# Performance work log

Measured on AMD Instinct MI355X. Metric: run time of the kernel, lower is better.

The kernel has to match this reference:

```python
import jax, jax.numpy as jnp
import numpy as np

H_DIM = 2048
D_FF = 4 * H_DIM
NUM_EXPERTS = 8
NUM_SHARED = 2
BATCH, SEQ = 2, 2048


def setup_inputs() -> dict:
    key = jax.random.key(0)
    ks = jax.random.split(key, 10)
    s = 0.02
    return {
        "x": jax.random.normal(ks[0], (BATCH, SEQ, H_DIM), dtype=jnp.float32),
        "ws_w1": jax.random.normal(ks[1], (NUM_SHARED, H_DIM, D_FF), dtype=jnp.float32) * s,
        "ws_b1": jnp.zeros((NUM_SHARED, D_FF), dtype=jnp.float32),
        "ws_w2": jax.random.normal(ks[2], (NUM_SHARED, D_FF, H_DIM), dtype=jnp.float32) * s,
        "ws_b2": jnp.zeros((NUM_SHARED, H_DIM), dtype=jnp.float32),
        "we_w1": jax.random.normal(ks[3], (NUM_EXPERTS, H_DIM, D_FF), dtype=jnp.float32) * s,
        "we_b1": jnp.zeros((NUM_EXPERTS, D_FF), dtype=jnp.float32),
        "we_w2": jax.random.normal(ks[4], (NUM_EXPERTS, D_FF, H_DIM), dtype=jnp.float32) * s,
        "we_b2": jnp.zeros((NUM_EXPERTS, H_DIM), dtype=jnp.float32),
        "wg": jax.random.normal(ks[5], (H_DIM, NUM_EXPERTS), dtype=jnp.float32) * s,
        "top_k": 2,
    }


def reference(x, ws_w1, ws_b1, ws_w2, ws_b2, we_w1, we_b1, we_w2, we_b2, wg, top_k):
    B, S, D = x.shape
    xt = x.reshape(-1, D)  # [T, D], T = B*S
    T = xt.shape[0]

    # ---- shared experts: sum over NUM_SHARED dense MLPs ----
    hs = jax.nn.relu(jnp.einsum('td,ndf->ntf', xt, ws_w1) + ws_b1[:, None, :])
    shared = jnp.einsum('ntf,nfd->td', hs, ws_w2) + ws_b2.sum(axis=0)  # [T, D]

    # ---- sparse top-k routed MoE ----
    logits = xt @ wg                       # [T, E] router logits
    probs = jax.nn.softmax(logits, axis=-1)
    topv, topi = jax.lax.top_k(probs, top_k)
    gates = jnp.zeros_like(probs).at[jnp.arange(T)[:, None], topi].set(topv)  # [T, E]

    moe = jnp.zeros_like(xt)
    for e in range(we_w1.shape[0]):  # small fixed expert count
        he = jax.nn.relu(xt @ we_w1[e] + we_b1[e])
        ye = he @ we_w2[e] + we_b2[e]
        moe = moe + gates[:, e:e + 1] * ye

    out = (shared + moe).reshape(B, S, D)
    return out, logits
```

## Files before the change

kernel.cpp:

```cpp
#include <hip/hip_runtime.h>

#define TOKENS 4096
#define HD 2048
#define FF 8192
#define NE 8
#define NS 2

typedef __attribute__((ext_vector_type(8))) short bf16x8;
typedef __attribute__((ext_vector_type(4))) float f32x4;

__device__ __forceinline__ unsigned rnd_bf(unsigned u) {
  return u + 0x7fffu + ((u >> 16) & 1u);
}
__device__ __forceinline__ unsigned short f2bf(float f) {
  unsigned u = __builtin_bit_cast(unsigned, f);
  return (unsigned short)(rnd_bf(u) >> 16);
}

#define GLDS16(gp, lp)                                                         \
  __builtin_amdgcn_global_load_lds(                                            \
      (const __attribute__((address_space(1))) unsigned*)(const void*)(gp),    \
      (__attribute__((address_space(3))) unsigned*)(lp), 16, 0, 0)

__global__ void cast_x_kernel(const float* __restrict__ x, unsigned short* __restrict__ xb) {
  const size_t i = ((size_t)blockIdx.x * 256 + threadIdx.x) * 4;
  float4 v = *(const float4*)(x + i);
  ushort4 o;
  o.x = f2bf(v.x); o.y = f2bf(v.y); o.z = f2bf(v.z); o.w = f2bf(v.w);
  *(ushort4*)(xb + i) = o;
}

__global__ void router_kernel(const float* __restrict__ x, const float* __restrict__ wg,
                              float* __restrict__ logits_out, int* __restrict__ topi,
                              float* __restrict__ topv, int* __restrict__ counts) {
  const int wave = threadIdx.x >> 6, lane = threadIdx.x & 63;
  const int t = blockIdx.x * 4 + wave;
  const float* xr = x + (size_t)t * HD;
  float acc[8];
#pragma unroll
  for (int e = 0; e < 8; ++e) acc[e] = 0.f;
  for (int d = lane; d < HD; d += 64) {
    const float xv = xr[d];
    const float4 w0 = *(const float4*)(wg + (size_t)d * 8);
    const float4 w1 = *(const float4*)(wg + (size_t)d * 8 + 4);
    acc[0] += xv * w0.x; acc[1] += xv * w0.y; acc[2] += xv * w0.z; acc[3] += xv * w0.w;
    acc[4] += xv * w1.x; acc[5] += xv * w1.y; acc[6] += xv * w1.z; acc[7] += xv * w1.w;
  }
#pragma unroll
  for (int e = 0; e < 8; ++e) {
#pragma unroll
    for (int off = 32; off > 0; off >>= 1) acc[e] += __shfl_xor(acc[e], off);
  }
  if (lane == 0) {
    *(float4*)(logits_out + (size_t)t * 8)     = make_float4(acc[0], acc[1], acc[2], acc[3]);
    *(float4*)(logits_out + (size_t)t * 8 + 4) = make_float4(acc[4], acc[5], acc[6], acc[7]);
    float mx = acc[0];
#pragma unroll
    for (int e = 1; e < 8; ++e) mx = fmaxf(mx, acc[e]);
    float p[8], s = 0.f;
#pragma unroll
    for (int e = 0; e < 8; ++e) { p[e] = expf(acc[e] - mx); s += p[e]; }
    const float inv = 1.f / s;
    int i1 = 0;
#pragma unroll
    for (int e = 1; e < 8; ++e) if (acc[e] > acc[i1]) i1 = e;
    int i2 = (i1 == 0) ? 1 : 0;
#pragma unroll
    for (int e = 0; e < 8; ++e) if (e != i1 && acc[e] > acc[i2]) i2 = e;
    topi[2 * t]     = i1; topv[2 * t]     = p[i1] * inv;
    topi[2 * t + 1] = i2; topv[2 * t + 1] = p[i2] * inv;
    atomicAdd(&counts[i1], 1);
    atomicAdd(&counts[i2], 1);
  }
}

__global__ void offs_kernel(const int* __restrict__ counts, int* __restrict__ offs,
                            int* __restrict__ cursors) {
  if (threadIdx.x == 0) {
    int r = 0;
    for (int e = 0; e < NE; ++e) { offs[e] = r; cursors[e] = r; r += counts[e]; }
  }
}

__global__ void gather_kernel(const unsigned short* __restrict__ xb,
                              const int* __restrict__ topi, const float* __restrict__ topv,
                              int* __restrict__ cursors, unsigned short* __restrict__ xg,
                              int* __restrict__ row_token, float* __restrict__ row_gate,
                              int* __restrict__ row_of) {
  const int wave = threadIdx.x >> 6, lane = threadIdx.x & 63;
  const int t = blockIdx.x * 4 + wave;
  const uint4* src = (const uint4*)(xb + (size_t)t * HD);
#pragma unroll
  for (int j = 0; j < 2; ++j) {
    const int e = topi[2 * t + j];
    int pos = 0;
    if (lane == 0) {
      pos = atomicAdd(&cursors[e], 1);
      row_token[pos] = t;
      row_gate[pos] = topv[2 * t + j];
      row_of[2 * t + j] = pos;
    }
    pos = __shfl(pos, 0);
    uint4* dst = (uint4*)(xg + (size_t)pos * HD);
#pragma unroll
    for (int c = lane; c < 256; c += 64) dst[c] = src[c];
  }
}

template <int K, int N>
__global__ __launch_bounds__(256) void pack_wt(const float* __restrict__ we,
                                               const float* __restrict__ ws,
                                               unsigned short* __restrict__ dstw) {
  const int e = blockIdx.z;
  const float* src = (e < NE) ? (we + (size_t)e * K * N) : (ws + (size_t)(e - NE) * K * N);
  unsigned short* dst = dstw + (size_t)e * K * N;
  const int nt = blockIdx.x * 64;
  const int kt = blockIdx.y * 64;
  __shared__ unsigned short t[64][73];
  const int tid = threadIdx.x;
  const int rr = tid >> 4, cc = (tid & 15) * 4;
#pragma unroll
  for (int i = 0; i < 4; ++i) {
    const int k = rr + i * 16;
    float4 v = *(const float4*)(src + (size_t)(kt + k) * N + nt + cc);
    t[k][cc + 0] = f2bf(v.x);
    t[k][cc + 1] = f2bf(v.y);
    t[k][cc + 2] = f2bf(v.z);
    t[k][cc + 3] = f2bf(v.w);
  }
  __syncthreads();
  const int nr = tid >> 2, kc = (tid & 3) * 16;
  unsigned u[8];
#pragma unroll
  for (int j = 0; j < 8; ++j)
    u[j] = (unsigned)t[kc + 2 * j][nr] | ((unsigned)t[kc + 2 * j + 1][nr] << 16);
  unsigned short* dp = dst + (size_t)(nt + nr) * K + kt + kc;
  uint4 v0; v0.x = u[0]; v0.y = u[1]; v0.z = u[2]; v0.w = u[3];
  uint4 v1; v1.x = u[4]; v1.y = u[5]; v1.z = u[6]; v1.w = u[7];
  *(uint4*)dp = v0;
  *(uint4*)(dp + 8) = v1;
}

template <int MS>
__device__ __forceinline__ void rd_a(bf16x8 (&d)[8], const unsigned short* base,
                                     int wr, int fr, int fq, int swz) {
#pragma unroll
  for (int mi = 0; mi < 4; ++mi)
#pragma unroll
    for (int ks = 0; ks < 2; ++ks)
      d[mi * 2 + ks] = *(const bf16x8*)(base + (wr * 128 + MS * 64 + mi * 16 + fr) * 64 +
                                        (((ks * 4 + fq) ^ swz) << 3));
}
template <int NSUB>
__device__ __forceinline__ void rd_b(bf16x8 (&d)[4], const unsigned short* base,
                                     int wc, int fr, int fq, int swz) {
#pragma unroll
  for (int ni = 0; ni < 2; ++ni)
#pragma unroll
    for (int ks = 0; ks < 2; ++ks)
      d[ni * 2 + ks] = *(const bf16x8*)(base + (wc * 64 + NSUB * 32 + ni * 16 + fr) * 64 +
                                        (((ks * 4 + fq) ^ swz) << 3));
}
template <int MS, int NSUB>
__device__ __forceinline__ void mm16(f32x4 (&acc)[8][4], const bf16x8 (&a)[8],
                                     const bf16x8 (&b)[4]) {
  __builtin_amdgcn_s_setprio(1);
#pragma unroll
  for (int mi = 0; mi < 4; ++mi)
#pragma unroll
    for (int ni = 0; ni < 2; ++ni)
#pragma unroll
      for (int ks = 0; ks < 2; ++ks)
        acc[MS * 4 + mi][NSUB * 2 + ni] = __builtin_amdgcn_mfma_f32_16x16x32_bf16(
            a[mi * 2 + ks], b[ni * 2 + ks], acc[MS * 4 + mi][NSUB * 2 + ni], 0, 0, 0);
  __builtin_amdgcn_s_setprio(0);
}
template <int MS>
__device__ __forceinline__ void mm32(f32x4 (&acc)[8][4], const bf16x8 (&a)[8],
                                     const bf16x8 (&b0)[4], const bf16x8 (&b1)[4]) {
  __builtin_amdgcn_s_setprio(1);
#pragma unroll
  for (int mi = 0; mi < 4; ++mi)
#pragma unroll
    for (int nn = 0; nn < 4; ++nn)
#pragma unroll
      for (int ks = 0; ks < 2; ++ks) {
        const bf16x8& bb = (nn < 2) ? b0[(nn & 1) * 2 + ks] : b1[(nn & 1) * 2 + ks];
        acc[MS * 4 + mi][nn] = __builtin_amdgcn_mfma_f32_16x16x32_bf16(
            a[mi * 2 + ks], bb, acc[MS * 4 + mi][nn], 0, 0, 0);
      }
  __builtin_amdgcn_s_setprio(0);
}

#define PH_BAR_PRE()                                                           \
  __builtin_amdgcn_sched_barrier(0);                                           \
  __builtin_amdgcn_s_barrier();                                                \
  asm volatile("s_waitcnt lgkmcnt(0)" ::: "memory");                           \
  __builtin_amdgcn_sched_barrier(0)
#define PH_BAR_POST()                                                          \
  __builtin_amdgcn_sched_barrier(0);                                           \
  __builtin_amdgcn_s_barrier()

__global__ __launch_bounds__(512, 2) void g1k(
    const unsigned short* __restrict__ Ash, const unsigned short* __restrict__ Art,
    const unsigned short* __restrict__ wt1,
    const float* __restrict__ bE, const float* __restrict__ bS,
    unsigned short* __restrict__ hout,
    const int* __restrict__ counts, const int* __restrict__ offs,
    int do_pack, const float* __restrict__ we_w2, const float* __restrict__ ws_w2,
    unsigned short* __restrict__ wt2) {
  constexpr int K = HD;
  constexpr int NBX = FF / 256;
  constexpr int NWG = NBX * 16;
  extern __shared__ unsigned short smem[];

  const int e = blockIdx.z;
  int M;
  const unsigned short* A;
  const float* bias;
  int hbase;
  if (e < NE) {
    M = counts[e];
    A = Art + (size_t)offs[e] * K;
    bias = bE + (size_t)e * FF;
    hbase = offs[e];
  } else {
    M = TOKENS;
    A = Ash;
    bias = bS + (size_t)(e - NE) * FF;
    hbase = 2 * TOKENS + (e - NE) * TOKENS;
  }
  const unsigned short* Bt = wt1 + (size_t)e * HD * FF;

  int flat = blockIdx.x + NBX * blockIdx.y;
  flat = (flat & 7) * (NWG >> 3) + (flat >> 3);
  const int m0 = (flat & 15) * 256;
  const int n0 = (flat >> 4) * 256;
  const int tid = threadIdx.x;

  if (m0 >= M) {
    if (!do_pack) return;
    int total = 0, prefix = 0;
    for (int e2 = 0; e2 < NE; ++e2) {
      int mb = (counts[e2] + 255) >> 8; if (mb > 16) mb = 16;
      const int inv = 32 * (16 - mb);
      if (e2 < e) prefix += inv;
      total += inv;
    }
    int mb_e = (counts[e] + 255) >> 8; if (mb_e > 16) mb_e = 16;
    const int m_idx = flat & 15, n_idx = flat >> 4;
    const int rank = prefix + n_idx * (16 - mb_e) + (m_idx - mb_e);
    unsigned short* ps = smem;
    const int NT = 10 * 128 * 32;
    for (int i = rank; i < NT; i += total) {
      const int e2 = i >> 12;
      const int rem = i & 4095;
      const int ktt = rem >> 5;
      const int ntt = rem & 31;
      const float* src = (e2 < NE) ? (we_w2 + (size_t)e2 * FF * HD)
                                   : (ws_w2 + (size_t)(e2 - NE) * FF * HD);
      unsigned short* dst = wt2 + (size_t)e2 * HD * FF;
      __syncthreads();
      {
        const int kk = tid >> 3, cc = (tid & 7) * 8;
        const float* sp = src + (size_t)(ktt * 64 + kk) * HD + ntt * 64 + cc;
        const float4 v0 = *(const float4*)sp;
        const float4 v1 = *(const float4*)(sp + 4);
        unsigned short* tp = ps + kk * 72 + cc;
        tp[0] = f2bf(v0.x); tp[1] = f2bf(v0.y); tp[2] = f2bf(v0.z); tp[3] = f2bf(v0.w);
        tp[4] = f2bf(v1.x); tp[5] = f2bf(v1.y); tp[6] = f2bf(v1.z); tp[7] = f2bf(v1.w);
      }
      __syncthreads();
      {
        const int nn = tid >> 3, kc = (tid & 7) * 8;
        unsigned u[4];
#pragma unroll
        for (int j = 0; j < 4; ++j)
          u[j] = (unsigned)ps[(kc + 2 * j) * 72 + nn] |
                 ((unsigned)ps[(kc + 2 * j + 1) * 72 + nn] << 16);
        uint4 v; v.x = u[0]; v.y = u[1]; v.z = u[2]; v.w = u[3];
        *(uint4*)(dst + (size_t)(ntt * 64 + nn) * FF + ktt * 64 + kc) = v;
      }
    }
    return;
  }

  const int wid = tid >> 6, ln = tid & 63;
  const int wr = wid >> 2, wc = wid & 3;
  const int fr = ln & 15, fq = ln >> 4;
  const int swz = fr & 7;
  const int lr8 = ln >> 3;
  const int lc8 = ln & 7;
  const int scol = (lc8 ^ lr8) << 3;
  const int wrA = wr * 128 + wc * 16;
  const int wcB = wc * 64 + wr * 16;

#define SA1(s, kt, b)                                                          \
  { const int r0_ = wrA + (s) * 64 + lr8;                                      \
    const unsigned short* s_ = A + (size_t)(m0 + r0_) * K + (kt) * 64 + scol;  \
    unsigned short* d_ = smem + (b) * 32768 + r0_ * 64 + lc8 * 8;              \
    GLDS16(s_, d_); GLDS16(s_ + (size_t)8 * K, d_ + 8 * 64); }
#define SB1(s, kt, b)                                                          \
  { const int r0_ = wcB + (s) * 32 + lr8;                                      \
    const unsigned short* s_ = Bt + (size_t)(n0 + r0_) * K + (kt) * 64 + scol; \
    unsigned short* d_ = smem + (b) * 32768 + 16384 + r0_ * 64 + lc8 * 8;      \
    GLDS16(s_, d_); GLDS16(s_ + (size_t)8 * K, d_ + 8 * 64); }

  f32x4 acc[8][4];
#pragma unroll
  for (int i = 0; i < 8; ++i)
#pragma unroll
    for (int j = 0; j < 4; ++j) acc[i][j] = (f32x4){0.f, 0.f, 0.f, 0.f};

  SA1(0, 0, 0); SA1(1, 0, 0); SB1(0, 0, 0); SB1(1, 0, 0);
  SA1(0, 1, 1); SA1(1, 1, 1); SB1(0, 1, 1); SB1(1, 1, 1);
  asm volatile("s_waitcnt vmcnt(8)" ::: "memory");
  __builtin_amdgcn_s_barrier();

  bf16x8 a0[8], a1[8], b0[4], b1[4];
  const int nkt = K / 64;
  for (int t = 0; t < nkt; ++t) {
    const int cur = t & 1;
    const int tp2 = (t + 2 < nkt) ? t + 2 : t;
    const unsigned short* As_c = smem + cur * 32768;
    const unsigned short* Bs_c = As_c + 16384;
    rd_a<0>(a0, As_c, wr, fr, fq, swz);
    rd_b<0>(b0, Bs_c, wc, fr, fq, swz);
    rd_b<1>(b1, Bs_c, wc, fr, fq, swz);
    asm volatile("s_waitcnt lgkmcnt(8)" ::: "memory");
    PH_BAR_PRE();
    mm32<0>(acc, a0, b0, b1);
    PH_BAR_POST();
    rd_a<1>(a1, As_c, wr, fr, fq, swz);
    SB1(0, tp2, cur); SB1(1, tp2, cur);
    PH_BAR_PRE();
    mm32<1>(acc, a1, b1, b0);
    __builtin_amdgcn_sched_barrier(0);
    SA1(0, tp2, cur); SA1(1, tp2, cur);
    __builtin_amdgcn_sched_barrier(0);
    asm volatile("s_waitcnt vmcnt(8)" ::: "memory");
    __builtin_amdgcn_s_barrier();
  }
#undef SA1
#undef SB1

#pragma unroll
  for (int nn = 0; nn < 4; ++nn) {
#pragma unroll
    for (int mm = 0; mm < 8; ++mm) {
      const int nsub_lo = (mm < 4) ? (nn >> 1) : 1 - (nn >> 1);
      const int col = n0 + wc * 64 + nsub_lo * 32 + (nn & 1) * 16 + fr;
      const float bb = bias[col];
#pragma unroll
      for (int j = 0; j < 4; ++j) {
        const int r = m0 + wr * 128 + (mm >> 2) * 64 + (mm & 3) * 16 + fq * 4 + j;
        if (r < M) {
          float v = acc[mm][nn][j] + bb;
          v = v > 0.f ? v : 0.f;
          hout[(size_t)(hbase + r) * FF + col] = f2bf(v);
        }
      }
    }
  }
}

__global__ __launch_bounds__(512, 2) void g2k(
    const unsigned short* __restrict__ hbuf, const unsigned short* __restrict__ wt2,
    const float* __restrict__ bE, const float* __restrict__ bS,
    float* __restrict__ ybuf,
    const int* __restrict__ counts, const int* __restrict__ offs) {
  constexpr int K = FF;
  constexpr int NBX = HD / 256;
  constexpr int NWG = NBX * 16;
  extern __shared__ unsigned short smem[];

  const int e = blockIdx.z;
  int M;
  const unsigned short* A;
  const float* bias;
  int hbase;
  if (e < NE) {
    M = counts[e];
    A = hbuf + (size_t)offs[e] * K;
    bias = bE + (size_t)e * HD;
    hbase = offs[e];
  } else {
    M = TOKENS;
    hbase = 2 * TOKENS + (e - NE) * TOKENS;
    A = hbuf + (size_t)hbase * K;
    bias = bS + (size_t)(e - NE) * HD;
  }
  const unsigned short* Bt = wt2 + (size_t)e * HD * FF;

  int flat = blockIdx.x + NBX * blockIdx.y;
  flat = (flat & 7) * (NWG >> 3) + (flat >> 3);
  const int m0 = (flat & 15) * 256;
  const int n0 = (flat >> 4) * 256;
  if (m0 >= M) return;

  const int tid = threadIdx.x;
  const int wid = tid >> 6, ln = tid & 63;
  const int wr = wid >> 2, wc = wid & 3;
  const int fr = ln & 15, fq = ln >> 4;
  const int swz = fr & 7;
  const int lr8 = ln >> 3;
  const int lc8 = ln & 7;
  const int scol = (lc8 ^ lr8) << 3;
  const int wrA = wr * 128 + wc * 16;
  const int wcB = wc * 64 + wr * 16;

#define SA2(s, kt, b)                                                          \
  { const int r0_ = wrA + (s) * 64 + lr8;                                      \
    const unsigned short* s_ = A + (size_t)(m0 + r0_) * K + (kt) * 64 + scol;  \
    unsigned short* d_ = smem + (b) * 32768 + r0_ * 64 + lc8 * 8;              \
    GLDS16(s_, d_); GLDS16(s_ + (size_t)8 * K, d_ + 8 * 64); }
#define SB2(s, kt, b)                                                          \
  { const int r0_ = wcB + (s) * 32 + lr8;                                      \
    const unsigned short* s_ = Bt + (size_t)(n0 + r0_) * K + (kt) * 64 + scol; \
    unsigned short* d_ = smem + (b) * 32768 + 16384 + r0_ * 64 + lc8 * 8;      \
    GLDS16(s_, d_); GLDS16(s_ + (size_t)8 * K, d_ + 8 * 64); }

  f32x4 acc[8][4];
#pragma unroll
  for (int i = 0; i < 8; ++i)
#pragma unroll
    for (int j = 0; j < 4; ++j) acc[i][j] = (f32x4){0.f, 0.f, 0.f, 0.f};

  SA2(0, 0, 0); SA2(1, 0, 0); SB2(0, 0, 0); SB2(1, 0, 0);
  SA2(0, 1, 1); SA2(1, 1, 1); SB2(0, 1, 1); SB2(1, 1, 1);
  asm volatile("s_waitcnt vmcnt(8)" ::: "memory");
  __builtin_amdgcn_s_barrier();

  bf16x8 a0[8], a1[8], b0[4], b1[4];
  const int nkt = K / 64;
  for (int t = 0; t < nkt; ++t) {
    const int cur = t & 1;
    const int tp2 = (t + 2 < nkt) ? t + 2 : t;
    const unsigned short* As_c = smem + cur * 32768;
    const unsigned short* Bs_c = As_c + 16384;
    rd_a<0>(a0, As_c, wr, fr, fq, swz);
    rd_b<0>(b0, Bs_c, wc, fr, fq, swz);
    rd_b<1>(b1, Bs_c, wc, fr, fq, swz);
    asm volatile("s_waitcnt lgkmcnt(8)" ::: "memory");
    PH_BAR_PRE();
    mm32<0>(acc, a0, b0, b1);
    PH_BAR_POST();
    rd_a<1>(a1, As_c, wr, fr, fq, swz);
    SB2(0, tp2, cur); SB2(1, tp2, cur);
    PH_BAR_PRE();
    mm32<1>(acc, a1, b1, b0);
    __builtin_amdgcn_sched_barrier(0);
    SA2(0, tp2, cur); SA2(1, tp2, cur);
    __builtin_amdgcn_sched_barrier(0);
    asm volatile("s_waitcnt vmcnt(8)" ::: "memory");
    __builtin_amdgcn_s_barrier();
  }
#undef SA2
#undef SB2

#pragma unroll
  for (int nn = 0; nn < 4; ++nn) {
#pragma unroll
    for (int mm = 0; mm < 8; ++mm) {
      const int nsub_lo = (mm < 4) ? (nn >> 1) : 1 - (nn >> 1);
      const int colw = wc * 64 + nsub_lo * 32 + (nn & 1) * 16 + fr;
      const float bb = bias[n0 + colw];
#pragma unroll
      for (int j = 0; j < 4; ++j) {
        const int r = m0 + wr * 128 + (mm >> 2) * 64 + (mm & 3) * 16 + fq * 4 + j;
        if (r < M)
          ybuf[(size_t)(hbase + r) * HD + n0 + colw] = acc[mm][nn][j] + bb;
      }
    }
  }
}

__global__ __launch_bounds__(256) void reduce_kernel(
    const float* __restrict__ ybuf, const int* __restrict__ row_of,
    const float* __restrict__ topv, float* __restrict__ out) {
  const int t = blockIdx.x;
  const int d = threadIdx.x * 8;
  const float g0 = topv[2 * t], g1 = topv[2 * t + 1];
  const float* y0 = ybuf + (size_t)row_of[2 * t] * HD + d;
  const float* y1 = ybuf + (size_t)row_of[2 * t + 1] * HD + d;
  const float* s0 = ybuf + (size_t)(2 * TOKENS + t) * HD + d;
  const float* s1 = ybuf + (size_t)(3 * TOKENS + t) * HD + d;
  float* o = out + (size_t)t * HD + d;
#pragma unroll
  for (int q = 0; q < 2; ++q) {
    const float4 a = *(const float4*)(s0 + q * 4);
    const float4 b = *(const float4*)(s1 + q * 4);
    const float4 c = *(const float4*)(y0 + q * 4);
    const float4 e = *(const float4*)(y1 + q * 4);
    float4 r;
    r.x = a.x + b.x + g0 * c.x + g1 * e.x;
    r.y = a.y + b.y + g0 * c.y + g1 * e.y;
    r.z = a.z + b.z + g0 * c.z + g1 * e.z;
    r.w = a.w + b.w + g0 * c.w + g1 * e.w;
    *(float4*)(o + q * 4) = r;
  }
}

__global__ __launch_bounds__(512, 2) void gemm8p(
    const unsigned short* __restrict__ hbuf,
    const unsigned short* __restrict__ wt,
    const float* __restrict__ bE, const float* __restrict__ bS,
    float* __restrict__ out,
    const int* __restrict__ counts, const int* __restrict__ offs,
    const int* __restrict__ row_token, const float* __restrict__ row_gate) {
  constexpr int K = FF;
  constexpr int NBX = HD / 256;
  constexpr int NWG = NBX * 16;
  extern __shared__ unsigned short smem[];

  const int e = blockIdx.z;
  const bool merged = (e == NE);
  int M;
  const unsigned short *A, *A2;
  const unsigned short *B, *B2;
  const float *bias, *bias2;
  const int* tok = nullptr;
  const float* gt = nullptr;

  if (!merged) {
    M = counts[e];
    const int off = offs[e];
    A = hbuf + (size_t)off * K;  A2 = A;
    tok = row_token + off; gt = row_gate + off;
    B = wt + (size_t)e * HD * FF;  B2 = B;
    bias = bE + (size_t)e * HD;  bias2 = bias;
  } else {
    M = TOKENS;
    A  = hbuf + (size_t)(2 * TOKENS) * K;
    A2 = hbuf + (size_t)(3 * TOKENS) * K;
    B  = wt + (size_t)NE * HD * FF;
    B2 = wt + (size_t)(NE + 1) * HD * FF;
    bias = bS;  bias2 = bS + HD;
  }

  int flat = blockIdx.x + NBX * blockIdx.y;
  flat = (flat & 7) * (NWG >> 3) + (flat >> 3);
  const int m0 = (flat & 15) * 256;
  const int n0 = (flat >> 4) * 256;
  if (m0 >= M) return;

  const int tid = threadIdx.x;
  const int wid = tid >> 6, ln = tid & 63;
  const int wr = wid >> 2, wc = wid & 3;
  const int fr = ln & 15, fq = ln >> 4;
  const int swz = fr & 7;
  const int lr8 = ln >> 3;
  const int lc8 = ln & 7;
  const int scol = (lc8 ^ lr8) << 3;
  const int wrA = wr * 128 + wc * 16;
  const int wcB = wc * 64 + wr * 16;

#define SAF(s, kt, b)                                                          \
  { int kl_ = (kt); const unsigned short* ab_ = A;                             \
    if (merged && kl_ >= 128) { ab_ = A2; kl_ -= 128; }                        \
    const int r0_ = wrA + (s) * 64 + lr8;                                      \
    const unsigned short* s_ = ab_ + (size_t)(m0 + r0_) * K + kl_ * 64 + scol; \
    unsigned short* d_ = smem + (b) * 32768 + r0_ * 64 + lc8 * 8;              \
    GLDS16(s_, d_); GLDS16(s_ + (size_t)8 * K, d_ + 8 * 64); }
#define SBF(s, kt, b)                                                          \
  { int kl_ = (kt); const unsigned short* bb_ = B;                             \
    if (merged && kl_ >= 128) { bb_ = B2; kl_ -= 128; }                        \
    const int r0_ = wcB + (s) * 32 + lr8;                                      \
    const unsigned short* s_ = bb_ + (size_t)(n0 + r0_) * K + kl_ * 64 + scol; \
    unsigned short* d_ = smem + (b) * 32768 + 16384 + r0_ * 64 + lc8 * 8;      \
    GLDS16(s_, d_); GLDS16(s_ + (size_t)8 * K, d_ + 8 * 64); }

  f32x4 acc[8][4];
#pragma unroll
  for (int i = 0; i < 8; ++i)
#pragma unroll
    for (int j = 0; j < 4; ++j) acc[i][j] = (f32x4){0.f, 0.f, 0.f, 0.f};

  SAF(0, 0, 0); SAF(1, 0, 0); SBF(0, 0, 0); SBF(1, 0, 0);
  SAF(0, 1, 1); SAF(1, 1, 1); SBF(0, 1, 1); SBF(1, 1, 1);
  asm volatile("s_waitcnt vmcnt(8)" ::: "memory");
  __builtin_amdgcn_s_barrier();

  bf16x8 a0[8], a1[8], b0[4], b1[4];
  const int nkt = merged ? 256 : 128;
  for (int t = 0; t < nkt; ++t) {
    const int cur = t & 1;
    const int tp2 = (t + 2 < nkt) ? t + 2 : t;
    const unsigned short* As_c = smem + cur * 32768;
    const unsigned short* Bs_c = As_c + 16384;
    rd_a<0>(a0, As_c, wr, fr, fq, swz);
    rd_b<0>(b0, Bs_c, wc, fr, fq, swz);
    asm volatile("s_waitcnt lgkmcnt(8)" ::: "memory");
    PH_BAR_PRE();
    mm16<0, 0>(acc, a0, b0);
    PH_BAR_POST();
    rd_b<1>(b1, Bs_c, wc, fr, fq, swz);
    SAF(0, tp2, cur); SBF(0, tp2, cur);
    PH_BAR_PRE();
    mm16<0, 1>(acc, a0, b1);
    PH_BAR_POST();
    rd_a<1>(a1, As_c, wr, fr, fq, swz);
    SBF(1, tp2, cur);
    PH_BAR_PRE();
    mm16<1, 1>(acc, a1, b1);
    PH_BAR_POST();
    SAF(1, tp2, cur);
    __builtin_amdgcn_sched_barrier(0);
    __builtin_amdgcn_s_barrier();
    __builtin_amdgcn_sched_barrier(0);
    mm16<1, 0>(acc, a1, b0);
    __builtin_amdgcn_sched_barrier(0);
    asm volatile("s_waitcnt vmcnt(8)" ::: "memory");
    __builtin_amdgcn_s_barrier();
  }
#undef SAF
#undef SBF

#pragma unroll
  for (int mm = 0; mm < 8; ++mm) {
#pragma unroll
    for (int j = 0; j < 4; ++j) {
      const int r = m0 + wr * 128 + (mm >> 2) * 64 + (mm & 3) * 16 + fq * 4 + j;
      if (r < M) {
        const int t = tok ? tok[r] : r;
        const float g = gt ? gt[r] : 1.f;
        float* orow = out + (size_t)t * HD + n0;
#pragma unroll
        for (int nn = 0; nn < 4; ++nn) {
          const int col = wc * 64 + (nn >> 1) * 32 + (nn & 1) * 16 + fr;
          float bb = bias[n0 + col];
          if (merged) bb += bias2[n0 + col];
          atomicAdd(orow + col, g * (acc[mm][nn][j] + bb));
        }
      }
    }
  }
}

extern "C" void kernel_launch(void* const* d_in, const int* in_sizes, int n_in,
                              void* d_out, int out_size, void* d_ws, size_t ws_size,
                              hipStream_t stream) {
  const float* x     = (const float*)d_in[0];
  const float* ws_w1 = (const float*)d_in[1];
  const float* ws_b1 = (const float*)d_in[2];
  const float* ws_w2 = (const float*)d_in[3];
  const float* ws_b2 = (const float*)d_in[4];
  const float* we_w1 = (const float*)d_in[5];
  const float* we_b1 = (const float*)d_in[6];
  const float* we_w2 = (const float*)d_in[7];
  const float* we_b2 = (const float*)d_in[8];
  const float* wg    = (const float*)d_in[9];

  float* out = (float*)d_out;
  float* logits = out + (size_t)TOKENS * HD;

  hipFuncSetAttribute(reinterpret_cast<const void*>(g1k),
                      hipFuncAttributeMaxDynamicSharedMemorySize, 131072);
  hipFuncSetAttribute(reinterpret_cast<const void*>(g2k),
                      hipFuncAttributeMaxDynamicSharedMemorySize, 131072);
  hipFuncSetAttribute(reinterpret_cast<const void*>(gemm8p),
                      hipFuncAttributeMaxDynamicSharedMemorySize, 131072);

  const size_t NEED2 = 990544000ull;
  char* ws = (char*)d_ws;

  if (ws_size >= NEED2) {
    unsigned short* wt1  = (unsigned short*)ws;
    unsigned short* wt2  = (unsigned short*)(ws + 335544320);
    unsigned short* xb   = (unsigned short*)(ws + 671088640);
    unsigned short* xg   = (unsigned short*)(ws + 687865856);
    unsigned short* hbuf = (unsigned short*)(ws + 721944576);
    char* ctrl = ws + 990380032;
    float* ybuf = (float*)ws;
    int*   row_token = (int*)(ctrl);
    float* row_gate  = (float*)(ctrl + 32768);
    int*   topi      = (int*)(ctrl + 65536);
    float* topv      = (float*)(ctrl + 98304);
    int*   counts    = (int*)(ctrl + 131072);
    int*   offs      = (int*)(ctrl + 131104);
    int*   cursors   = (int*)(ctrl + 131136);
    int*   row_of    = (int*)(ctrl + 131168);

    hipMemsetAsync(counts, 0, NE * sizeof(int), stream);
    cast_x_kernel<<<8192, 256, 0, stream>>>(x, xb);
    router_kernel<<<1024, 256, 0, stream>>>(x, wg, logits, topi, topv, counts);
    offs_kernel<<<1, 64, 0, stream>>>(counts, offs, cursors);
    gather_kernel<<<1024, 256, 0, stream>>>(xb, topi, topv, cursors, xg,
                                            row_token, row_gate, row_of);
    pack_wt<HD, FF><<<dim3(FF / 64, HD / 64, 10), 256, 0, stream>>>(we_w1, ws_w1, wt1);
    g1k<<<dim3(32, 16, 10), 512, 131072, stream>>>(
        xb, xg, wt1, we_b1, ws_b1, hbuf, counts, offs, 1, we_w2, ws_w2, wt2);
    g2k<<<dim3(8, 16, 10), 512, 131072, stream>>>(
        hbuf, wt2, we_b2, ws_b2, ybuf, counts, offs);
    reduce_kernel<<<TOKENS, 256, 0, stream>>>(ybuf, row_of, topv, out);
  } else {
    unsigned short* wt   = (unsigned short*)ws;
    unsigned short* xb   = (unsigned short*)(ws + 335544320);
    unsigned short* xg   = (unsigned short*)(ws + 352321536);
    unsigned short* hbuf = (unsigned short*)(ws + 386400256);
    char* ctrl = ws + 654835712;
    int*   row_token = (int*)(ctrl);
    float* row_gate  = (float*)(ctrl + 32768);
    int*   topi      = (int*)(ctrl + 65536);
    float* topv      = (float*)(ctrl + 98304);
    int*   counts    = (int*)(ctrl + 131072);
    int*   offs      = (int*)(ctrl + 131104);
    int*   cursors   = (int*)(ctrl + 131136);
    int*   row_of    = (int*)(ctrl + 131168);

    hipMemsetAsync(out, 0, (size_t)TOKENS * HD * sizeof(float), stream);
    hipMemsetAsync(counts, 0, NE * sizeof(int), stream);

    cast_x_kernel<<<8192, 256, 0, stream>>>(x, xb);
    router_kernel<<<1024, 256, 0, stream>>>(x, wg, logits, topi, topv, counts);
    offs_kernel<<<1, 64, 0, stream>>>(counts, offs, cursors);
    gather_kernel<<<1024, 256, 0, stream>>>(xb, topi, topv, cursors, xg,
                                            row_token, row_gate, row_of);

    pack_wt<HD, FF><<<dim3(FF / 64, HD / 64, 10), 256, 0, stream>>>(we_w1, ws_w1, wt);
    g1k<<<dim3(32, 16, 10), 512, 131072, stream>>>(
        xb, xg, wt, we_b1, ws_b1, hbuf, counts, offs, 0, nullptr, nullptr, nullptr);
    pack_wt<FF, HD><<<dim3(HD / 64, FF / 64, 10), 256, 0, stream>>>(we_w2, ws_w2, wt);
    gemm8p<<<dim3(8, 16, 9), 512, 131072, stream>>>(
        hbuf, wt, we_b2, ws_b2, out, counts, offs, row_token, row_gate);
  }

  (void)in_sizes; (void)n_in; (void)out_size; (void)ws_size;
}
```

Before: 2.033 ms.

## Restructure GEMM k-loop into four interleaved MFMA quadrants with prefetched LDS reads

Replaces the two-phase mm32 schedule in both the up- and down-projection GEMMs with a shared kloop that issues four 16-wide MFMA quadrants, interleaving LDS fragment reads and global-to-LDS loads between them. The A0/B0 fragments for the next k-tile are read at the end of the current iteration, so LDS latency overlaps the last MFMA block. The aim is to cut exposed LDS-read and barrier stalls. It changes the waitcnt/barrier ordering, which risks races or a worse schedule, and the epilogue column mapping is simplified to match the new accumulator layout.

Result: faster. 1.914 ms (-5.9%).

```diff
diff --git a/kernel.cpp b/kernel.cpp
--- a/kernel.cpp
+++ b/kernel.cpp
@@ -175,22 +175,6 @@
             a[mi * 2 + ks], b[ni * 2 + ks], acc[MS * 4 + mi][NSUB * 2 + ni], 0, 0, 0);
   __builtin_amdgcn_s_setprio(0);
 }
-template <int MS>
-__device__ __forceinline__ void mm32(f32x4 (&acc)[8][4], const bf16x8 (&a)[8],
-                                     const bf16x8 (&b0)[4], const bf16x8 (&b1)[4]) {
-  __builtin_amdgcn_s_setprio(1);
-#pragma unroll
-  for (int mi = 0; mi < 4; ++mi)
-#pragma unroll
-    for (int nn = 0; nn < 4; ++nn)
-#pragma unroll
-      for (int ks = 0; ks < 2; ++ks) {
-        const bf16x8& bb = (nn < 2) ? b0[(nn & 1) * 2 + ks] : b1[(nn & 1) * 2 + ks];
-        acc[MS * 4 + mi][nn] = __builtin_amdgcn_mfma_f32_16x16x32_bf16(
-            a[mi * 2 + ks], bb, acc[MS * 4 + mi][nn], 0, 0, 0);
-      }
-  __builtin_amdgcn_s_setprio(0);
-}
 
 #define PH_BAR_PRE()                                                           \
   __builtin_amdgcn_sched_barrier(0);                                           \
@@ -200,6 +184,61 @@
 #define PH_BAR_POST()                                                          \
   __builtin_amdgcn_sched_barrier(0);                                           \
   __builtin_amdgcn_s_barrier()
+
+template <int K>
+__device__ __forceinline__ void kloop(
+    const unsigned short* __restrict__ A, const unsigned short* __restrict__ Bt,
+    unsigned short* smem, int m0, int n0, f32x4 (&acc)[8][4],
+    int wr, int wc, int fr, int fq, int swz,
+    int wrA, int wcB, int lr8, int lc8, int scol) {
+#define SAK(s, kt, b)                                                          \
+  { const int r0_ = wrA + (s) * 64 + lr8;                                      \
+    const unsigned short* s_ = A + (size_t)(m0 + r0_) * K + (kt) * 64 + scol;  \
+    unsigned short* d_ = smem + (b) * 32768 + r0_ * 64 + lc8 * 8;              \
+    GLDS16(s_, d_); GLDS16(s_ + (size_t)8 * K, d_ + 8 * 64); }
+#define SBK(s, kt, b)                                                          \
+  { const int r0_ = wcB + (s) * 32 + lr8;                                      \
+    const unsigned short* s_ = Bt + (size_t)(n0 + r0_) * K + (kt) * 64 + scol; \
+    unsigned short* d_ = smem + (b) * 32768 + 16384 + r0_ * 64 + lc8 * 8;      \
+    GLDS16(s_, d_); GLDS16(s_ + (size_t)8 * K, d_ + 8 * 64); }
+
+  SAK(0, 0, 0); SAK(1, 0, 0); SBK(0, 0, 0); SBK(1, 0, 0);
+  SAK(0, 1, 1); SAK(1, 1, 1); SBK(0, 1, 1); SBK(1, 1, 1);
+  asm volatile("s_waitcnt vmcnt(8)" ::: "memory");
+  __builtin_amdgcn_s_barrier();
+
+  bf16x8 a0[8], a1[8], b0[4], b1[4];
+  rd_a<0>(a0, smem, wr, fr, fq, swz);
+  rd_b<0>(b0, smem + 16384, wc, fr, fq, swz);
+
+  const int nkt = K / 64;
+  for (int t = 0; t < nkt; ++t) {
+    const int cur = t & 1;
+    const int tp2 = (t + 2 < nkt) ? t + 2 : t;
+    const unsigned short* As_c = smem + cur * 32768;
+    const unsigned short* Bs_c = As_c + 16384;
+    const unsigned short* As_n = smem + (cur ^ 1) * 32768;
+    const unsigned short* Bs_n = As_n + 16384;
+    rd_b<1>(b1, Bs_c, wc, fr, fq, swz);
+    mm16<0, 0>(acc, a0, b0);
+    rd_a<1>(a1, As_c, wr, fr, fq, swz);
+    mm16<0, 1>(acc, a0, b1);
+    asm volatile("s_waitcnt lgkmcnt(0)" ::: "memory");
+    __builtin_amdgcn_s_barrier();
+    __builtin_amdgcn_sched_barrier(0);
+    SAK(0, tp2, cur); SBK(0, tp2, cur);
+    mm16<1, 0>(acc, a1, b0);
+    asm volatile("s_waitcnt vmcnt(4)" ::: "memory");
+    __builtin_amdgcn_s_barrier();
+    __builtin_amdgcn_sched_barrier(0);
+    rd_a<0>(a0, As_n, wr, fr, fq, swz);
+    rd_b<0>(b0, Bs_n, wc, fr, fq, swz);
+    SAK(1, tp2, cur); SBK(1, tp2, cur);
+    mm16<1, 1>(acc, a1, b1);
+  }
+#undef SAK
+#undef SBK
+}
 
 __global__ __launch_bounds__(512, 2) void g1k(
     const unsigned short* __restrict__ Ash, const unsigned short* __restrict__ Art,
@@ -295,61 +334,19 @@
   const int wrA = wr * 128 + wc * 16;
   const int wcB = wc * 64 + wr * 16;
 
-#define SA1(s, kt, b)                                                          \
-  { const int r0_ = wrA + (s) * 64 + lr8;                                      \
-    const unsigned short* s_ = A + (size_t)(m0 + r0_) * K + (kt) * 64 + scol;  \
-    unsigned short* d_ = smem + (b) * 32768 + r0_ * 64 + lc8 * 8;              \
-    GLDS16(s_, d_); GLDS16(s_ + (size_t)8 * K, d_ + 8 * 64); }
-#define SB1(s, kt, b)                                                          \
-  { const int r0_ = wcB + (s) * 32 + lr8;                                      \
-    const unsigned short* s_ = Bt + (size_t)(n0 + r0_) * K + (kt) * 64 + scol; \
-    unsigned short* d_ = smem + (b) * 32768 + 16384 + r0_ * 64 + lc8 * 8;      \
-    GLDS16(s_, d_); GLDS16(s_ + (size_t)8 * K, d_ + 8 * 64); }
-
   f32x4 acc[8][4];
 #pragma unroll
   for (int i = 0; i < 8; ++i)
 #pragma unroll
     for (int j = 0; j < 4; ++j) acc[i][j] = (f32x4){0.f, 0.f, 0.f, 0.f};
 
-  SA1(0, 0, 0); SA1(1, 0, 0); SB1(0, 0, 0); SB1(1, 0, 0);
-  SA1(0, 1, 1); SA1(1, 1, 1); SB1(0, 1, 1); SB1(1, 1, 1);
-  asm volatile("s_waitcnt vmcnt(8)" ::: "memory");
-  __builtin_amdgcn_s_barrier();
-
-  bf16x8 a0[8], a1[8], b0[4], b1[4];
-  const int nkt = K / 64;
-  for (int t = 0; t < nkt; ++t) {
-    const int cur = t & 1;
-    const int tp2 = (t + 2 < nkt) ? t + 2 : t;
-    const unsigned short* As_c = smem + cur * 32768;
-    const unsigned short* Bs_c = As_c + 16384;
-    rd_a<0>(a0, As_c, wr, fr, fq, swz);
-    rd_b<0>(b0, Bs_c, wc, fr, fq, swz);
-    rd_b<1>(b1, Bs_c, wc, fr, fq, swz);
-    asm volatile("s_waitcnt lgkmcnt(8)" ::: "memory");
-    PH_BAR_PRE();
-    mm32<0>(acc, a0, b0, b1);
-    PH_BAR_POST();
-    rd_a<1>(a1, As_c, wr, fr, fq, swz);
-    SB1(0, tp2, cur); SB1(1, tp2, cur);
-    PH_BAR_PRE();
-    mm32<1>(acc, a1, b1, b0);
-    __builtin_amdgcn_sched_barrier(0);
-    SA1(0, tp2, cur); SA1(1, tp2, cur);
-    __builtin_amdgcn_sched_barrier(0);
-    asm volatile("s_waitcnt vmcnt(8)" ::: "memory");
-    __builtin_amdgcn_s_barrier();
-  }
-#undef SA1
-#undef SB1
+  kloop<K>(A, Bt, smem, m0, n0, acc, wr, wc, fr, fq, swz, wrA, wcB, lr8, lc8, scol);
 
 #pragma unroll
   for (int nn = 0; nn < 4; ++nn) {
 #pragma unroll
     for (int mm = 0; mm < 8; ++mm) {
-      const int nsub_lo = (mm < 4) ? (nn >> 1) : 1 - (nn >> 1);
-      const int col = n0 + wc * 64 + nsub_lo * 32 + (nn & 1) * 16 + fr;
+      const int col = n0 + wc * 64 + (nn >> 1) * 32 + (nn & 1) * 16 + fr;
       const float bb = bias[col];
 #pragma unroll
       for (int j = 0; j < 4; ++j) {
@@ -409,61 +406,19 @@
   const int wrA = wr * 128 + wc * 16;
   const int wcB = wc * 64 + wr * 16;
 
-#define SA2(s, kt, b)                                                          \
-  { const int r0_ = wrA + (s) * 64 + lr8;                                      \
-    const unsigned short* s_ = A + (size_t)(m0 + r0_) * K + (kt) * 64 + scol;  \
-    unsigned short* d_ = smem + (b) * 32768 + r0_ * 64 + lc8 * 8;              \
-    GLDS16(s_, d_); GLDS16(s_ + (size_t)8 * K, d_ + 8 * 64); }
-#define SB2(s, kt, b)                                                          \
-  { const int r0_ = wcB + (s) * 32 + lr8;                                      \
-    const unsigned short* s_ = Bt + (size_t)(n0 + r0_) * K + (kt) * 64 + scol; \
-    unsigned short* d_ = smem + (b) * 32768 + 16384 + r0_ * 64 + lc8 * 8;      \
-    GLDS16(s_, d_); GLDS16(s_ + (size_t)8 * K, d_ + 8 * 64); }
-
   f32x4 acc[8][4];
 #pragma unroll
   for (int i = 0; i < 8; ++i)
 #pragma unroll
     for (int j = 0; j < 4; ++j) acc[i][j] = (f32x4){0.f, 0.f, 0.f, 0.f};
 
-  SA2(0, 0, 0); SA2(1, 0, 0); SB2(0, 0, 0); SB2(1, 0, 0);
-  SA2(0, 1, 1); SA2(1, 1, 1); SB2(0, 1, 1); SB2(1, 1, 1);
-  asm volatile("s_waitcnt vmcnt(8)" ::: "memory");
-  __builtin_amdgcn_s_barrier();
-
-  bf16x8 a0[8], a1[8], b0[4], b1[4];
-  const int nkt = K / 64;
-  for (int t = 0; t < nkt; ++t) {
-    const int cur = t & 1;
-    const int tp2 = (t + 2 < nkt) ? t + 2 : t;
-    const unsigned short* As_c = smem + cur * 32768;
-    const unsigned short* Bs_c = As_c + 16384;
-    rd_a<0>(a0, As_c, wr, fr, fq, swz);
-    rd_b<0>(b0, Bs_c, wc, fr, fq, swz);
-    rd_b<1>(b1, Bs_c, wc, fr, fq, swz);
-    asm volatile("s_waitcnt lgkmcnt(8)" ::: "memory");
-    PH_BAR_PRE();
-    mm32<0>(acc, a0, b0, b1);
-    PH_BAR_POST();
-    rd_a<1>(a1, As_c, wr, fr, fq, swz);
-    SB2(0, tp2, cur); SB2(1, tp2, cur);
-    PH_BAR_PRE();
-    mm32<1>(acc, a1, b1, b0);
-    __builtin_amdgcn_sched_barrier(0);
-    SA2(0, tp2, cur); SA2(1, tp2, cur);
-    __builtin_amdgcn_sched_barrier(0);
-    asm volatile("s_waitcnt vmcnt(8)" ::: "memory");
-    __builtin_amdgcn_s_barrier();
-  }
-#undef SA2
-#undef SB2
+  kloop<K>(A, Bt, smem, m0, n0, acc, wr, wc, fr, fq, swz, wrA, wcB, lr8, lc8, scol);
 
 #pragma unroll
   for (int nn = 0; nn < 4; ++nn) {
 #pragma unroll
     for (int mm = 0; mm < 8; ++mm) {
-      const int nsub_lo = (mm < 4) ? (nn >> 1) : 1 - (nn >> 1);
-      const int colw = wc * 64 + nsub_lo * 32 + (nn & 1) * 16 + fr;
+      const int colw = wc * 64 + (nn >> 1) * 32 + (nn & 1) * 16 + fr;
       const float bb = bias[n0 + colw];
 #pragma unroll
       for (int j = 0; j < 4; ++j) {
```
